# Kernel optimization log

Measured on AMD Instinct MI355X. Metric: run time of the kernel, lower is better.

## Reference

```python
import jax, jax.numpy as jnp
import numpy as np

N_NODES = 100000
N_EDGES = 3200000
N_GRAPHS = 256
IN_CH, EDGE_CH, HID, N_CLS = 11, 22, 64, 2


def setup_inputs() -> dict:
    key = jax.random.key(0)
    ks = jax.random.split(key, 16)
    s = 0.1
    return {
        "x": jax.random.normal(ks[0], (N_NODES, IN_CH), jnp.float32),
        "edge_attr": jax.random.normal(ks[1], (N_EDGES, EDGE_CH), jnp.float32),
        "edge_index": jax.random.randint(ks[2], (2, N_EDGES), 0, N_NODES, jnp.int64),
        "batch": jnp.sort(jax.random.randint(ks[3], (N_NODES,), 0, N_GRAPHS, jnp.int64)),
        # fc_edge: Linear(edge_ch -> in_ch)
        "we": jax.random.normal(ks[4], (IN_CH, EDGE_CH), jnp.float32) * s,
        "be": jnp.zeros((IN_CH,), jnp.float32),
        # SAGEConv i: lin_l (neighbors, with bias), lin_r (root, no bias)
        "l1w": jax.random.normal(ks[5], (HID, IN_CH), jnp.float32) * s,
        "l1b": jnp.zeros((HID,), jnp.float32),
        "r1w": jax.random.normal(ks[6], (HID, IN_CH), jnp.float32) * s,
        "l2w": jax.random.normal(ks[7], (HID, HID), jnp.float32) * s,
        "l2b": jnp.zeros((HID,), jnp.float32),
        "r2w": jax.random.normal(ks[8], (HID, HID), jnp.float32) * s,
        "l3w": jax.random.normal(ks[9], (HID, HID), jnp.float32) * s,
        "l3b": jnp.zeros((HID,), jnp.float32),
        "r3w": jax.random.normal(ks[10], (HID, HID), jnp.float32) * s,
        # final classifier
        "wf": jax.random.normal(ks[11], (N_CLS, HID), jnp.float32) * s,
        "bf": jnp.zeros((N_CLS,), jnp.float32),
    }


def _sage(x, src, dst, lw, lb, rw):
    # mean aggregation of source-node features at destination nodes
    agg = jax.ops.segment_sum(x[src], dst, num_segments=N_NODES)
    deg = jax.ops.segment_sum(jnp.ones((src.shape[0],), x.dtype), dst, num_segments=N_NODES)
    mean = agg / jnp.maximum(deg, 1.0)[:, None]
    return mean @ lw.T + lb + x @ rw.T


def reference(x, edge_attr, edge_index, batch, we, be,
              l1w, l1b, r1w, l2w, l2b, r2w, l3w, l3b, r3w, wf, bf):
    src, dst = edge_index[0], edge_index[1]
    # per-edge correction scatter-added to source nodes
    ec = edge_attr @ we.T + be                       # [E, in_ch]
    x = x.at[src].add(ec)                            # [N, in_ch]
    x = jax.nn.relu(_sage(x, src, dst, l1w, l1b, r1w))
    x = jax.nn.relu(_sage(x, src, dst, l2w, l2b, r2w))
    x = jax.nn.relu(_sage(x, src, dst, l3w, l3b, r3w))
    # global mean pool per graph
    psum = jax.ops.segment_sum(x, batch, num_segments=N_GRAPHS)
    cnt = jax.ops.segment_sum(jnp.ones((x.shape[0],), x.dtype), batch, num_segments=N_GRAPHS)
    pooled = psum / jnp.maximum(cnt, 1.0)[:, None]   # [G, hid]
    # dropout is identity in eval mode
    return pooled @ wf.T + bf                        # [G, num_classes]
```

## Files before the change

kernel.cpp:

```cpp
#include <hip/hip_runtime.h>
#include <stdint.h>

#define IN_CH 11
#define EDGE_CH 22
#define HID 64
#define N_CLS 2
#define N_GRAPHS 256

#define BK_SHIFT 8
#define BK_NODES 256
#define MAXBUK 512
#define L1_CHUNK 4096
#define L2_CAP 16384

#define SRC_SHIFT 22
#define DST_SHIFT 17

__global__ void prehist_kernel(const int* __restrict__ src, const int* __restrict__ dst,
                               int* __restrict__ bc_src, int* __restrict__ bc_dst,
                               int E, int nbuk) {
    __shared__ int h_s[MAXBUK], h_d[MAXBUK];
    int t = threadIdx.x;
    for (int i = t; i < MAXBUK; i += 256) { h_s[i] = 0; h_d[i] = 0; }
    __syncthreads();
    int per = (E + gridDim.x - 1) / gridDim.x;
    int lo = blockIdx.x * per, hi = min(E, lo + per);
    for (int i = lo + t; i < hi; i += 256) {
        atomicAdd(&h_s[src[i] >> BK_SHIFT], 1);
        atomicAdd(&h_d[dst[i] >> BK_SHIFT], 1);
    }
    __syncthreads();
    for (int i = t; i < nbuk; i += 256) {
        if (h_s[i]) atomicAdd(&bc_src[i], h_s[i]);
        if (h_d[i]) atomicAdd(&bc_dst[i], h_d[i]);
    }
}

__global__ void bucket_scan_kernel(const int* __restrict__ bc_src, const int* __restrict__ bc_dst,
                                   int* __restrict__ boff_src, int* __restrict__ boff_dst,
                                   int* __restrict__ gcur_src, int* __restrict__ gcur_dst,
                                   int* __restrict__ off_src, int* __restrict__ off_dst,
                                   int nbuk, int N, int E) {
    __shared__ int a[MAXBUK], b[MAXBUK];
    int t = threadIdx.x;
    int ca = (t < nbuk) ? bc_src[t] : 0;
    int cb = (t < nbuk) ? bc_dst[t] : 0;
    a[t] = ca; b[t] = cb;
    __syncthreads();
    for (int d = 1; d < MAXBUK; d <<= 1) {
        int ua = (t >= d) ? a[t - d] : 0;
        int ub = (t >= d) ? b[t - d] : 0;
        __syncthreads();
        a[t] += ua; b[t] += ub;
        __syncthreads();
    }
    if (t < nbuk) {
        int ea = a[t] - ca, eb = b[t] - cb;
        boff_src[t] = ea; gcur_src[t] = ea;
        boff_dst[t] = eb; gcur_dst[t] = eb;
    }
    if (t == 0) {
        boff_src[nbuk] = E; boff_dst[nbuk] = E;
        off_src[N] = E; off_dst[N] = E;
    }
}

__global__ void binscatter_kernel(const int* __restrict__ src, const int* __restrict__ dst,
                                  int* __restrict__ gcur_src, int* __restrict__ gcur_dst,
                                  uint32_t* __restrict__ bin_src, uint32_t* __restrict__ bin_dst,
                                  int E, int nbuk) {
    __shared__ int h_s[MAXBUK], h_d[MAXBUK];
    __shared__ int off_s[MAXBUK], off_d[MAXBUK];
    __shared__ int cur_s[MAXBUK], cur_d[MAXBUK];
    __shared__ int base_s[MAXBUK], base_d[MAXBUK];
    __shared__ uint32_t st_s[L1_CHUNK], st_d[L1_CHUNK];
    __shared__ unsigned short bk_s[L1_CHUNK], bk_d[L1_CHUNK];

    int t = threadIdx.x;
    int e0 = blockIdx.x * L1_CHUNK;
    int ecnt = min(E - e0, L1_CHUNK);

    h_s[t] = 0; h_d[t] = 0;
    __syncthreads();
    for (int i = t; i < ecnt; i += 512) {
        atomicAdd(&h_s[src[e0 + i] >> BK_SHIFT], 1);
        atomicAdd(&h_d[dst[e0 + i] >> BK_SHIFT], 1);
    }
    __syncthreads();
    int cs = h_s[t], cd = h_d[t];
    for (int d = 1; d < MAXBUK; d <<= 1) {
        int us = (t >= d) ? h_s[t - d] : 0;
        int ud = (t >= d) ? h_d[t - d] : 0;
        __syncthreads();
        h_s[t] += us; h_d[t] += ud;
        __syncthreads();
    }
    int ex_s = h_s[t] - cs, ex_d = h_d[t] - cd;
    off_s[t] = ex_s; cur_s[t] = ex_s;
    off_d[t] = ex_d; cur_d[t] = ex_d;
    if (cs > 0) base_s[t] = atomicAdd(&gcur_src[t], cs);
    if (cd > 0) base_d[t] = atomicAdd(&gcur_dst[t], cd);
    __syncthreads();
    for (int i = t; i < ecnt; i += 512) {
        int e = e0 + i;
        int s = src[e], d = dst[e];
        int bs = s >> BK_SHIFT, bd = d >> BK_SHIFT;
        int ps = atomicAdd(&cur_s[bs], 1);
        st_s[ps] = ((uint32_t)(s & (BK_NODES - 1)) << SRC_SHIFT) | (uint32_t)e;
        bk_s[ps] = (unsigned short)bs;
        int pd = atomicAdd(&cur_d[bd], 1);
        st_d[pd] = ((uint32_t)(d & (BK_NODES - 1)) << DST_SHIFT) | (uint32_t)s;
        bk_d[pd] = (unsigned short)bd;
    }
    __syncthreads();
    for (int i = t; i < ecnt; i += 512) {
        int b1 = bk_s[i];
        bin_src[base_s[b1] + i - off_s[b1]] = st_s[i];
        int b2 = bk_d[i];
        bin_dst[base_d[b2] + i - off_d[b2]] = st_d[i];
    }
}

__global__ void bucket_csr_kernel(const uint32_t* __restrict__ bin_src,
                                  const int* __restrict__ boff_src,
                                  int* __restrict__ src_edge, int* __restrict__ off_src,
                                  const uint32_t* __restrict__ bin_dst,
                                  const int* __restrict__ boff_dst,
                                  int* __restrict__ dst_srcid, int* __restrict__ off_dst,
                                  int nbuk, int N) {
    bool is_dst = blockIdx.x >= (unsigned)nbuk;
    int b = is_dst ? (blockIdx.x - nbuk) : blockIdx.x;
    const uint32_t* bin = is_dst ? bin_dst : bin_src;
    const int* boff = is_dst ? boff_dst : boff_src;
    int* outp = is_dst ? dst_srcid : src_edge;
    int* offo = is_dst ? off_dst : off_src;
    int shift = is_dst ? DST_SHIFT : SRC_SHIFT;
    uint32_t mask = (1u << shift) - 1;

    __shared__ int hist[BK_NODES];
    __shared__ int cursor[BK_NODES];
    __shared__ uint32_t stage[L2_CAP];

    int t = threadIdx.x;
    int base = boff[b];
    int cnt = boff[b + 1] - base;
    int n0 = b << BK_SHIFT;
    int NL = min(N - n0, BK_NODES);

    hist[t] = 0;
    __syncthreads();
    for (int i = t; i < cnt; i += 256) {
        atomicAdd(&hist[bin[base + i] >> shift], 1);
    }
    __syncthreads();
    int c = hist[t];
    for (int d = 1; d < BK_NODES; d <<= 1) {
        int u = (t >= d) ? hist[t - d] : 0;
        __syncthreads();
        hist[t] += u;
        __syncthreads();
    }
    int excl = hist[t] - c;
    cursor[t] = excl;
    if (t < NL) offo[n0 + t] = base + excl;
    __syncthreads();
    for (int i = t; i < cnt; i += 256) {
        uint32_t w = bin[base + i];
        int local = (int)(w >> shift);
        int pos = atomicAdd(&cursor[local], 1);
        uint32_t payload = w & mask;
        if (pos < L2_CAP) stage[pos] = payload;
        else outp[base + pos] = (int)payload;
    }
    __syncthreads();
    int lim = min(cnt, L2_CAP);
    for (int i = t; i < lim; i += 256) outp[base + i] = (int)stage[i];
}

__global__ void ea_gather_kernel(const float* __restrict__ ea,
                                 const int* __restrict__ off_src,
                                 const int* __restrict__ src_edge,
                                 float* __restrict__ agg_ea, int N) {
    int wave = (blockIdx.x * blockDim.x + threadIdx.x) >> 6;
    int lane = threadIdx.x & 63;
    if (wave >= N) return;
    int beg = off_src[wave], end = off_src[wave + 1];
    int j = lane >> 5;
    int c = lane & 31;
    float acc = 0.0f;
    if (c < EDGE_CH) {
        for (int i = beg + j; i < end; i += 2) {
            int e = src_edge[i];
            acc += ea[(long)e * EDGE_CH + c];
        }
    }
    acc += __shfl_xor(acc, 32, 64);
    if (lane < EDGE_CH) agg_ea[(long)wave * EDGE_CH + lane] = acc;
}

__global__ void x0_update_kernel(const float* __restrict__ x,
                                 const float* __restrict__ agg_ea,
                                 const int* __restrict__ off_src,
                                 const float* __restrict__ we,
                                 const float* __restrict__ be,
                                 float* __restrict__ x0, int N) {
    __shared__ float s_we[IN_CH * EDGE_CH];
    __shared__ float s_be[IN_CH];
    for (int i = threadIdx.x; i < IN_CH * EDGE_CH; i += blockDim.x) s_we[i] = we[i];
    if (threadIdx.x < IN_CH) s_be[threadIdx.x] = be[threadIdx.x];
    __syncthreads();
    int n = blockIdx.x * blockDim.x + threadIdx.x;
    if (n >= N) return;
    float a[EDGE_CH];
#pragma unroll
    for (int k = 0; k < EDGE_CH; ++k) a[k] = agg_ea[(long)n * EDGE_CH + k];
    float cnt = (float)(off_src[n + 1] - off_src[n]);
#pragma unroll
    for (int o = 0; o < IN_CH; ++o) {
        float acc = x[(long)n * IN_CH + o] + cnt * s_be[o];
#pragma unroll
        for (int k = 0; k < EDGE_CH; ++k) acc += a[k] * s_we[o * EDGE_CH + k];
        x0[(long)n * IN_CH + o] = acc;
    }
}

__global__ void agg11_kernel(const float* __restrict__ h,
                             const int* __restrict__ off_dst,
                             const int* __restrict__ srcid,
                             float* __restrict__ mean, int N) {
    int wave = (blockIdx.x * blockDim.x + threadIdx.x) >> 6;
    int lane = threadIdx.x & 63;
    if (wave >= N) return;
    int beg = off_dst[wave], end = off_dst[wave + 1];
    int j = lane >> 4;
    int c = lane & 15;
    float acc = 0.0f;
    if (c < IN_CH) {
        for (int i = beg + j; i < end; i += 4) {
            acc += h[(long)srcid[i] * IN_CH + c];
        }
    }
    acc += __shfl_xor(acc, 16, 64);
    acc += __shfl_xor(acc, 32, 64);
    if (lane < IN_CH) {
        float inv = 1.0f / fmaxf((float)(end - beg), 1.0f);
        mean[(long)wave * IN_CH + lane] = acc * inv;
    }
}

__global__ void agg64_kernel(const float* __restrict__ h,
                             const int* __restrict__ off_dst,
                             const int* __restrict__ srcid,
                             float* __restrict__ mean, int N) {
    int wave = (blockIdx.x * blockDim.x + threadIdx.x) >> 6;
    int lane = threadIdx.x & 63;
    if (wave >= N) return;
    int beg = off_dst[wave], end = off_dst[wave + 1];
    float a0 = 0.0f, a1 = 0.0f;
    int i = beg;
    for (; i + 1 < end; i += 2) {
        int s0 = srcid[i], s1 = srcid[i + 1];
        a0 += h[(long)s0 * HID + lane];
        a1 += h[(long)s1 * HID + lane];
    }
    if (i < end) a0 += h[(long)srcid[i] * HID + lane];
    float inv = 1.0f / fmaxf((float)(end - beg), 1.0f);
    mean[(long)wave * HID + lane] = (a0 + a1) * inv;
}

template <int CIN>
__global__ void update_kernel(const float* __restrict__ h_in,
                              const float* __restrict__ mean,
                              const float* __restrict__ lw,
                              const float* __restrict__ lb,
                              const float* __restrict__ rw,
                              float* __restrict__ h_out, int N) {
    __shared__ float s_lw[CIN][HID];
    __shared__ float s_rw[CIN][HID];
    __shared__ float s_lb[HID];
    __shared__ float s_hin[4][CIN];
    __shared__ float s_mean[4][CIN];
    for (int i = threadIdx.x; i < HID * CIN; i += blockDim.x) {
        int o = i / CIN, c = i % CIN;
        s_lw[c][o] = lw[i];
        s_rw[c][o] = rw[i];
    }
    if (threadIdx.x < HID) s_lb[threadIdx.x] = lb[threadIdx.x];
    __syncthreads();
    int sub = threadIdx.x >> 6, lane = threadIdx.x & 63;
    int groups = (N + 3) >> 2;
    for (int g = blockIdx.x; g < groups; g += gridDim.x) {
        int n = g * 4 + sub;
        bool valid = n < N;
        if (valid && lane < CIN) {
            s_hin[sub][lane] = h_in[(long)n * CIN + lane];
            s_mean[sub][lane] = mean[(long)n * CIN + lane];
        }
        __syncthreads();
        if (valid) {
            float acc = s_lb[lane];
#pragma unroll
            for (int c2 = 0; c2 < CIN; ++c2)
                acc += s_mean[sub][c2] * s_lw[c2][lane] + s_hin[sub][c2] * s_rw[c2][lane];
            h_out[(long)n * HID + lane] = fmaxf(acc, 0.0f);
        }
        __syncthreads();
    }
}

__global__ void pool_kernel(const float* __restrict__ h,
                            const int* __restrict__ batch,
                            float* __restrict__ psum,
                            float* __restrict__ pcnt,
                            int N, int chunk) {
    int lane = threadIdx.x;
    int n0 = blockIdx.x * chunk;
    int n1 = min(n0 + chunk, N);
    float acc = 0.0f, cnt = 0.0f;
    int cur = -1;
    for (int n = n0; n < n1; ++n) {
        int g = batch[n];
        if (g != cur) {
            if (cur >= 0) {
                atomicAdd(&psum[(long)cur * HID + lane], acc);
                if (lane == 0) atomicAdd(&pcnt[cur], cnt);
            }
            cur = g;
            acc = 0.0f;
            cnt = 0.0f;
        }
        acc += h[(long)n * HID + lane];
        cnt += 1.0f;
    }
    if (cur >= 0) {
        atomicAdd(&psum[(long)cur * HID + lane], acc);
        if (lane == 0) atomicAdd(&pcnt[cur], cnt);
    }
}

__global__ void final_kernel(const float* __restrict__ psum,
                             const float* __restrict__ pcnt,
                             const float* __restrict__ wf,
                             const float* __restrict__ bf,
                             float* __restrict__ out, int G) {
    int g = blockIdx.x * blockDim.x + threadIdx.x;
    if (g < G) {
        float inv = 1.0f / fmaxf(pcnt[g], 1.0f);
        float o0 = bf[0], o1 = bf[1];
#pragma unroll
        for (int c = 0; c < HID; ++c) {
            float p = psum[(long)g * HID + c] * inv;
            o0 += p * wf[c];
            o1 += p * wf[HID + c];
        }
        out[g * N_CLS + 0] = o0;
        out[g * N_CLS + 1] = o1;
    }
}

extern "C" void kernel_launch(void* const* d_in, const int* in_sizes, int n_in,
                              void* d_out, int out_size, void* d_ws, size_t ws_size,
                              hipStream_t stream) {
    const float* x         = (const float*)d_in[0];
    const float* edge_attr = (const float*)d_in[1];
    const int*   edge_idx  = (const int*)d_in[2];
    const int*   batch     = (const int*)d_in[3];
    const float* we  = (const float*)d_in[4];
    const float* be  = (const float*)d_in[5];
    const float* l1w = (const float*)d_in[6];
    const float* l1b = (const float*)d_in[7];
    const float* r1w = (const float*)d_in[8];
    const float* l2w = (const float*)d_in[9];
    const float* l2b = (const float*)d_in[10];
    const float* r2w = (const float*)d_in[11];
    const float* l3w = (const float*)d_in[12];
    const float* l3b = (const float*)d_in[13];
    const float* r3w = (const float*)d_in[14];
    const float* wf  = (const float*)d_in[15];
    const float* bf  = (const float*)d_in[16];

    const int E = in_sizes[2] / 2;
    const int N = in_sizes[3];
    const int* src = edge_idx;
    const int* dst = edge_idx + E;
    const int nbuk = (N + BK_NODES - 1) >> BK_SHIFT;

    char* p = (char*)d_ws;
    int* off_src   = (int*)p;            p += (size_t)(N + 1) * 4;
    int* off_dst   = (int*)p;            p += (size_t)(N + 1) * 4;
    int* bc_src    = (int*)p;            p += (size_t)MAXBUK * 4;
    int* bc_dst    = (int*)p;            p += (size_t)MAXBUK * 4;
    int* boff_src  = (int*)p;            p += (size_t)(MAXBUK + 1) * 4;
    int* boff_dst  = (int*)p;            p += (size_t)(MAXBUK + 1) * 4;
    int* gcur_src  = (int*)p;            p += (size_t)MAXBUK * 4;
    int* gcur_dst  = (int*)p;            p += (size_t)MAXBUK * 4;
    int* src_edge  = (int*)p;            p += (size_t)E * 4;
    int* dst_srcid = (int*)p;            p += (size_t)E * 4;
    float* x0      = (float*)p;          p += (size_t)N * IN_CH * 4;
    float* tmpM    = (float*)p;          p += (size_t)N * HID * 4;
    float* bufA    = (float*)p;          p += (size_t)N * HID * 4;
    float* bufB    = (float*)p;          p += (size_t)N * HID * 4;
    float* psum    = (float*)p;          p += (size_t)N_GRAPHS * HID * 4;
    float* pcnt    = (float*)p;          p += (size_t)N_GRAPHS * 4;

    uint32_t* bin_src = (uint32_t*)bufA;
    uint32_t* bin_dst = bin_src + E;

    const int NW = (N + 3) / 4;

    hipMemsetAsync(bc_src, 0, (size_t)MAXBUK * 2 * 4, stream);
    prehist_kernel<<<512, 256, 0, stream>>>(src, dst, bc_src, bc_dst, E, nbuk);
    bucket_scan_kernel<<<1, MAXBUK, 0, stream>>>(bc_src, bc_dst, boff_src, boff_dst,
                                                 gcur_src, gcur_dst, off_src, off_dst,
                                                 nbuk, N, E);
    binscatter_kernel<<<(E + L1_CHUNK - 1) / L1_CHUNK, 512, 0, stream>>>(
        src, dst, gcur_src, gcur_dst, bin_src, bin_dst, E, nbuk);
    bucket_csr_kernel<<<2 * nbuk, 256, 0, stream>>>(
        bin_src, boff_src, src_edge, off_src,
        bin_dst, boff_dst, dst_srcid, off_dst, nbuk, N);

    ea_gather_kernel<<<NW, 256, 0, stream>>>(edge_attr, off_src, src_edge, tmpM, N);
    x0_update_kernel<<<(N + 255) / 256, 256, 0, stream>>>(x, tmpM, off_src, we, be, x0, N);

    agg11_kernel<<<NW, 256, 0, stream>>>(x0, off_dst, dst_srcid, tmpM, N);
    update_kernel<IN_CH><<<2048, 256, 0, stream>>>(x0, tmpM, l1w, l1b, r1w, bufA, N);

    agg64_kernel<<<NW, 256, 0, stream>>>(bufA, off_dst, dst_srcid, tmpM, N);
    update_kernel<HID><<<2048, 256, 0, stream>>>(bufA, tmpM, l2w, l2b, r2w, bufB, N);

    agg64_kernel<<<NW, 256, 0, stream>>>(bufB, off_dst, dst_srcid, tmpM, N);
    update_kernel<HID><<<2048, 256, 0, stream>>>(bufB, tmpM, l3w, l3b, r3w, bufA, N);

    hipMemsetAsync(psum, 0, (size_t)(N_GRAPHS * HID + N_GRAPHS) * 4, stream);
    {
        int pb = 256;
        int chunk = (N + pb - 1) / pb;
        pool_kernel<<<pb, 64, 0, stream>>>(bufA, batch, psum, pcnt, N, chunk);
    }
    final_kernel<<<(N_GRAPHS + 255) / 256, 256, 0, stream>>>(psum, pcnt, wf, bf,
                                                             (float*)d_out, N_GRAPHS);
}
```

Baseline: 1.508 ms.

## Fuse edge-attr aggregation into bucket pass and fuse SAGE aggregation with update

Removes the src-side CSR build and instead aggregates edge attributes per source bucket directly in shared memory with LDS atomics, fused with the x0 linear update. Mean aggregation and the dense update of each SAGE layer are merged into a single kernel, so the intermediate mean buffer never goes through global memory. Gather loops are unrolled further for more memory-level parallelism, and the pool grid is widened. The trade-offs are heavy LDS atomic contention in the bucket kernel, fewer blocks for the hidden layers because of larger shared-memory use, and barriers inside the fused loops.

New measurement: 1.440 ms. 1.05x faster.

```diff
diff --git a/kernel.cpp b/kernel.cpp
--- a/kernel.cpp
+++ b/kernel.cpp
@@ -39,7 +39,7 @@
 __global__ void bucket_scan_kernel(const int* __restrict__ bc_src, const int* __restrict__ bc_dst,
                                    int* __restrict__ boff_src, int* __restrict__ boff_dst,
                                    int* __restrict__ gcur_src, int* __restrict__ gcur_dst,
-                                   int* __restrict__ off_src, int* __restrict__ off_dst,
+                                   int* __restrict__ off_dst,
                                    int nbuk, int N, int E) {
     __shared__ int a[MAXBUK], b[MAXBUK];
     int t = threadIdx.x;
@@ -61,7 +61,7 @@
     }
     if (t == 0) {
         boff_src[nbuk] = E; boff_dst[nbuk] = E;
-        off_src[N] = E; off_dst[N] = E;
+        off_dst[N] = E;
     }
 }
 
@@ -121,36 +121,26 @@
     }
 }
 
-__global__ void bucket_csr_kernel(const uint32_t* __restrict__ bin_src,
-                                  const int* __restrict__ boff_src,
-                                  int* __restrict__ src_edge, int* __restrict__ off_src,
-                                  const uint32_t* __restrict__ bin_dst,
+__global__ void bucket_csr_kernel(const uint32_t* __restrict__ bin_dst,
                                   const int* __restrict__ boff_dst,
                                   int* __restrict__ dst_srcid, int* __restrict__ off_dst,
                                   int nbuk, int N) {
-    bool is_dst = blockIdx.x >= (unsigned)nbuk;
-    int b = is_dst ? (blockIdx.x - nbuk) : blockIdx.x;
-    const uint32_t* bin = is_dst ? bin_dst : bin_src;
-    const int* boff = is_dst ? boff_dst : boff_src;
-    int* outp = is_dst ? dst_srcid : src_edge;
-    int* offo = is_dst ? off_dst : off_src;
-    int shift = is_dst ? DST_SHIFT : SRC_SHIFT;
-    uint32_t mask = (1u << shift) - 1;
-
+    int b = blockIdx.x;
     __shared__ int hist[BK_NODES];
     __shared__ int cursor[BK_NODES];
     __shared__ uint32_t stage[L2_CAP];
 
     int t = threadIdx.x;
-    int base = boff[b];
-    int cnt = boff[b + 1] - base;
+    int base = boff_dst[b];
+    int cnt = boff_dst[b + 1] - base;
     int n0 = b << BK_SHIFT;
     int NL = min(N - n0, BK_NODES);
+    uint32_t mask = (1u << DST_SHIFT) - 1;
 
     hist[t] = 0;
     __syncthreads();
     for (int i = t; i < cnt; i += 256) {
-        atomicAdd(&hist[bin[base + i] >> shift], 1);
+        atomicAdd(&hist[bin_dst[base + i] >> DST_SHIFT], 1);
     }
     __syncthreads();
     int c = hist[t];
@@ -162,147 +152,198 @@
     }
     int excl = hist[t] - c;
     cursor[t] = excl;
-    if (t < NL) offo[n0 + t] = base + excl;
+    if (t < NL) off_dst[n0 + t] = base + excl;
     __syncthreads();
     for (int i = t; i < cnt; i += 256) {
-        uint32_t w = bin[base + i];
-        int local = (int)(w >> shift);
+        uint32_t w = bin_dst[base + i];
+        int local = (int)(w >> DST_SHIFT);
         int pos = atomicAdd(&cursor[local], 1);
         uint32_t payload = w & mask;
         if (pos < L2_CAP) stage[pos] = payload;
-        else outp[base + pos] = (int)payload;
+        else dst_srcid[base + pos] = (int)payload;
     }
     __syncthreads();
     int lim = min(cnt, L2_CAP);
-    for (int i = t; i < lim; i += 256) outp[base + i] = (int)stage[i];
-}
-
-__global__ void ea_gather_kernel(const float* __restrict__ ea,
-                                 const int* __restrict__ off_src,
-                                 const int* __restrict__ src_edge,
-                                 float* __restrict__ agg_ea, int N) {
-    int wave = (blockIdx.x * blockDim.x + threadIdx.x) >> 6;
-    int lane = threadIdx.x & 63;
-    if (wave >= N) return;
-    int beg = off_src[wave], end = off_src[wave + 1];
-    int j = lane >> 5;
-    int c = lane & 31;
-    float acc = 0.0f;
-    if (c < EDGE_CH) {
-        for (int i = beg + j; i < end; i += 2) {
-            int e = src_edge[i];
-            acc += ea[(long)e * EDGE_CH + c];
-        }
-    }
-    acc += __shfl_xor(acc, 32, 64);
-    if (lane < EDGE_CH) agg_ea[(long)wave * EDGE_CH + lane] = acc;
-}
-
-__global__ void x0_update_kernel(const float* __restrict__ x,
-                                 const float* __restrict__ agg_ea,
-                                 const int* __restrict__ off_src,
+    for (int i = t; i < lim; i += 256) dst_srcid[base + i] = (int)stage[i];
+}
+
+__global__ void bucket_ea_kernel(const uint32_t* __restrict__ bin_src,
+                                 const int* __restrict__ boff_src,
+                                 const float* __restrict__ ea,
+                                 const float* __restrict__ x,
                                  const float* __restrict__ we,
                                  const float* __restrict__ be,
-                                 float* __restrict__ x0, int N) {
+                                 float* __restrict__ x0,
+                                 int nbuk, int N) {
+    __shared__ float s_ea[BK_NODES][EDGE_CH];
+    __shared__ int s_cnt[BK_NODES];
     __shared__ float s_we[IN_CH * EDGE_CH];
     __shared__ float s_be[IN_CH];
-    for (int i = threadIdx.x; i < IN_CH * EDGE_CH; i += blockDim.x) s_we[i] = we[i];
-    if (threadIdx.x < IN_CH) s_be[threadIdx.x] = be[threadIdx.x];
-    __syncthreads();
-    int n = blockIdx.x * blockDim.x + threadIdx.x;
-    if (n >= N) return;
-    float a[EDGE_CH];
-#pragma unroll
-    for (int k = 0; k < EDGE_CH; ++k) a[k] = agg_ea[(long)n * EDGE_CH + k];
-    float cnt = (float)(off_src[n + 1] - off_src[n]);
-#pragma unroll
-    for (int o = 0; o < IN_CH; ++o) {
-        float acc = x[(long)n * IN_CH + o] + cnt * s_be[o];
-#pragma unroll
-        for (int k = 0; k < EDGE_CH; ++k) acc += a[k] * s_we[o * EDGE_CH + k];
-        x0[(long)n * IN_CH + o] = acc;
-    }
-}
-
-__global__ void agg11_kernel(const float* __restrict__ h,
+    int t = threadIdx.x;
+    int b = blockIdx.x;
+    int base = boff_src[b];
+    int cnt = boff_src[b + 1] - base;
+    int n0 = b << BK_SHIFT;
+    int NL = min(N - n0, BK_NODES);
+
+    for (int i = t; i < IN_CH * EDGE_CH; i += 256) s_we[i] = we[i];
+    if (t < IN_CH) s_be[t] = be[t];
+    s_cnt[t] = 0;
+#pragma unroll
+    for (int c = 0; c < EDGE_CH; ++c) s_ea[t][c] = 0.0f;
+    __syncthreads();
+
+    const float2* ea2 = (const float2*)ea;
+    const uint32_t emask = (1u << SRC_SHIFT) - 1;
+    for (int i = t; i < cnt; i += 256) {
+        uint32_t w = bin_src[base + i];
+        int local = (int)(w >> SRC_SHIFT);
+        long eid = (long)(w & emask);
+        atomicAdd(&s_cnt[local], 1);
+        const float2* row = ea2 + eid * (EDGE_CH / 2);
+        float2 v[EDGE_CH / 2];
+#pragma unroll
+        for (int c = 0; c < EDGE_CH / 2; ++c) v[c] = row[c];
+#pragma unroll
+        for (int c = 0; c < EDGE_CH / 2; ++c) {
+            atomicAdd(&s_ea[local][2 * c], v[c].x);
+            atomicAdd(&s_ea[local][2 * c + 1], v[c].y);
+        }
+    }
+    __syncthreads();
+
+    if (t < NL) {
+        int n = n0 + t;
+        float cntf = (float)s_cnt[t];
+        float a[EDGE_CH];
+#pragma unroll
+        for (int c = 0; c < EDGE_CH; ++c) a[c] = s_ea[t][c];
+#pragma unroll
+        for (int o = 0; o < IN_CH; ++o) {
+            float acc = x[(long)n * IN_CH + o] + cntf * s_be[o];
+#pragma unroll
+            for (int c = 0; c < EDGE_CH; ++c) acc += a[c] * s_we[o * EDGE_CH + c];
+            x0[(long)n * IN_CH + o] = acc;
+        }
+    }
+}
+
+__global__ void layer1_fused(const float* __restrict__ x0,
                              const int* __restrict__ off_dst,
                              const int* __restrict__ srcid,
-                             float* __restrict__ mean, int N) {
-    int wave = (blockIdx.x * blockDim.x + threadIdx.x) >> 6;
-    int lane = threadIdx.x & 63;
-    if (wave >= N) return;
-    int beg = off_dst[wave], end = off_dst[wave + 1];
-    int j = lane >> 4;
-    int c = lane & 15;
-    float acc = 0.0f;
-    if (c < IN_CH) {
-        for (int i = beg + j; i < end; i += 4) {
-            acc += h[(long)srcid[i] * IN_CH + c];
-        }
-    }
-    acc += __shfl_xor(acc, 16, 64);
-    acc += __shfl_xor(acc, 32, 64);
-    if (lane < IN_CH) {
-        float inv = 1.0f / fmaxf((float)(end - beg), 1.0f);
-        mean[(long)wave * IN_CH + lane] = acc * inv;
-    }
-}
-
-__global__ void agg64_kernel(const float* __restrict__ h,
-                             const int* __restrict__ off_dst,
-                             const int* __restrict__ srcid,
-                             float* __restrict__ mean, int N) {
-    int wave = (blockIdx.x * blockDim.x + threadIdx.x) >> 6;
-    int lane = threadIdx.x & 63;
-    if (wave >= N) return;
-    int beg = off_dst[wave], end = off_dst[wave + 1];
-    float a0 = 0.0f, a1 = 0.0f;
-    int i = beg;
-    for (; i + 1 < end; i += 2) {
-        int s0 = srcid[i], s1 = srcid[i + 1];
-        a0 += h[(long)s0 * HID + lane];
-        a1 += h[(long)s1 * HID + lane];
-    }
-    if (i < end) a0 += h[(long)srcid[i] * HID + lane];
-    float inv = 1.0f / fmaxf((float)(end - beg), 1.0f);
-    mean[(long)wave * HID + lane] = (a0 + a1) * inv;
-}
-
-template <int CIN>
-__global__ void update_kernel(const float* __restrict__ h_in,
-                              const float* __restrict__ mean,
-                              const float* __restrict__ lw,
-                              const float* __restrict__ lb,
-                              const float* __restrict__ rw,
-                              float* __restrict__ h_out, int N) {
-    __shared__ float s_lw[CIN][HID];
-    __shared__ float s_rw[CIN][HID];
+                             const float* __restrict__ lw,
+                             const float* __restrict__ lb,
+                             const float* __restrict__ rw,
+                             float* __restrict__ h_out, int N) {
+    __shared__ float s_lw[IN_CH][HID];
+    __shared__ float s_rw[IN_CH][HID];
     __shared__ float s_lb[HID];
-    __shared__ float s_hin[4][CIN];
-    __shared__ float s_mean[4][CIN];
-    for (int i = threadIdx.x; i < HID * CIN; i += blockDim.x) {
-        int o = i / CIN, c = i % CIN;
+    __shared__ float s_mean[4][IN_CH];
+    __shared__ float s_hin[4][IN_CH];
+    for (int i = threadIdx.x; i < HID * IN_CH; i += 256) {
+        int o = i / IN_CH, c = i % IN_CH;
         s_lw[c][o] = lw[i];
         s_rw[c][o] = rw[i];
     }
     if (threadIdx.x < HID) s_lb[threadIdx.x] = lb[threadIdx.x];
-    __syncthreads();
+
+    int sub = threadIdx.x >> 6, lane = threadIdx.x & 63;
+    int j = lane >> 4, c = lane & 15;
+    int groups = (N + 3) >> 2;
+    for (int g = blockIdx.x; g < groups; g += gridDim.x) {
+        int n = g * 4 + sub;
+        bool valid = n < N;
+        int beg = 0, end = 0;
+        if (valid) { beg = off_dst[n]; end = off_dst[n + 1]; }
+        float a0 = 0.f, a1 = 0.f, a2 = 0.f, a3 = 0.f;
+        int i = beg;
+        if (valid && c < IN_CH) {
+            for (; i + 15 < end; i += 16) {
+                int s0 = srcid[i + j];
+                int s1 = srcid[i + j + 4];
+                int s2 = srcid[i + j + 8];
+                int s3 = srcid[i + j + 12];
+                a0 += x0[(long)s0 * IN_CH + c];
+                a1 += x0[(long)s1 * IN_CH + c];
+                a2 += x0[(long)s2 * IN_CH + c];
+                a3 += x0[(long)s3 * IN_CH + c];
+            }
+            for (; i + j < end; i += 4) a0 += x0[(long)srcid[i + j] * IN_CH + c];
+        }
+        float acc = (a0 + a1) + (a2 + a3);
+        acc += __shfl_xor(acc, 16, 64);
+        acc += __shfl_xor(acc, 32, 64);
+        if (valid && lane < IN_CH) {
+            float inv = 1.0f / fmaxf((float)(end - beg), 1.0f);
+            s_mean[sub][lane] = acc * inv;
+            s_hin[sub][lane] = x0[(long)n * IN_CH + lane];
+        }
+        __syncthreads();
+        if (valid) {
+            float oacc = s_lb[lane];
+#pragma unroll
+            for (int cc = 0; cc < IN_CH; ++cc)
+                oacc += s_mean[sub][cc] * s_lw[cc][lane] + s_hin[sub][cc] * s_rw[cc][lane];
+            h_out[(long)n * HID + lane] = fmaxf(oacc, 0.0f);
+        }
+        __syncthreads();
+    }
+}
+
+__global__ void layer_hid_fused(const float* __restrict__ h_in,
+                                const int* __restrict__ off_dst,
+                                const int* __restrict__ srcid,
+                                const float* __restrict__ lw,
+                                const float* __restrict__ lb,
+                                const float* __restrict__ rw,
+                                float* __restrict__ h_out, int N) {
+    __shared__ float s_lw[HID][HID];
+    __shared__ float s_rw[HID][HID];
+    __shared__ float s_lb[HID];
+    __shared__ float s_mean[4][HID];
+    __shared__ float s_hin[4][HID];
+    for (int i = threadIdx.x; i < HID * HID; i += 256) {
+        int o = i >> 6, c = i & 63;
+        s_lw[c][o] = lw[i];
+        s_rw[c][o] = rw[i];
+    }
+    if (threadIdx.x < HID) s_lb[threadIdx.x] = lb[threadIdx.x];
+
     int sub = threadIdx.x >> 6, lane = threadIdx.x & 63;
     int groups = (N + 3) >> 2;
     for (int g = blockIdx.x; g < groups; g += gridDim.x) {
         int n = g * 4 + sub;
         bool valid = n < N;
-        if (valid && lane < CIN) {
-            s_hin[sub][lane] = h_in[(long)n * CIN + lane];
-            s_mean[sub][lane] = mean[(long)n * CIN + lane];
-        }
-        __syncthreads();
+        int beg = 0, end = 0;
+        if (valid) { beg = off_dst[n]; end = off_dst[n + 1]; }
+        float a0 = 0.f, a1 = 0.f, a2 = 0.f, a3 = 0.f;
+        float a4 = 0.f, a5 = 0.f, a6 = 0.f, a7 = 0.f;
+        int i = beg;
+        for (; i + 7 < end; i += 8) {
+            int s0 = srcid[i], s1 = srcid[i + 1], s2 = srcid[i + 2], s3 = srcid[i + 3];
+            int s4 = srcid[i + 4], s5 = srcid[i + 5], s6 = srcid[i + 6], s7 = srcid[i + 7];
+            a0 += h_in[(long)s0 * HID + lane];
+            a1 += h_in[(long)s1 * HID + lane];
+            a2 += h_in[(long)s2 * HID + lane];
+            a3 += h_in[(long)s3 * HID + lane];
+            a4 += h_in[(long)s4 * HID + lane];
+            a5 += h_in[(long)s5 * HID + lane];
+            a6 += h_in[(long)s6 * HID + lane];
+            a7 += h_in[(long)s7 * HID + lane];
+        }
+        for (; i < end; ++i) a0 += h_in[(long)srcid[i] * HID + lane];
         if (valid) {
-            float acc = s_lb[lane];
-#pragma unroll
-            for (int c2 = 0; c2 < CIN; ++c2)
-                acc += s_mean[sub][c2] * s_lw[c2][lane] + s_hin[sub][c2] * s_rw[c2][lane];
-            h_out[(long)n * HID + lane] = fmaxf(acc, 0.0f);
+            float inv = 1.0f / fmaxf((float)(end - beg), 1.0f);
+            s_mean[sub][lane] = (((a0 + a1) + (a2 + a3)) + ((a4 + a5) + (a6 + a7))) * inv;
+            s_hin[sub][lane] = h_in[(long)n * HID + lane];
+        }
+        __syncthreads();
+        if (valid) {
+            float oacc = s_lb[lane];
+#pragma unroll
+            for (int cc = 0; cc < HID; ++cc)
+                oacc += s_mean[sub][cc] * s_lw[cc][lane] + s_hin[sub][cc] * s_rw[cc][lane];
+            h_out[(long)n * HID + lane] = fmaxf(oacc, 0.0f);
         }
         __syncthreads();
     }
@@ -386,7 +427,6 @@
     const int nbuk = (N + BK_NODES - 1) >> BK_SHIFT;
 
     char* p = (char*)d_ws;
-    int* off_src   = (int*)p;            p += (size_t)(N + 1) * 4;
     int* off_dst   = (int*)p;            p += (size_t)(N + 1) * 4;
     int* bc_src    = (int*)p;            p += (size_t)MAXBUK * 4;
     int* bc_dst    = (int*)p;            p += (size_t)MAXBUK * 4;
@@ -394,46 +434,38 @@
     int* boff_dst  = (int*)p;            p += (size_t)(MAXBUK + 1) * 4;
     int* gcur_src  = (int*)p;            p += (size_t)MAXBUK * 4;
     int* gcur_dst  = (int*)p;            p += (size_t)MAXBUK * 4;
-    int* src_edge  = (int*)p;            p += (size_t)E * 4;
     int* dst_srcid = (int*)p;            p += (size_t)E * 4;
     float* x0      = (float*)p;          p += (size_t)N * IN_CH * 4;
-    float* tmpM    = (float*)p;          p += (size_t)N * HID * 4;
     float* bufA    = (float*)p;          p += (size_t)N * HID * 4;
     float* bufB    = (float*)p;          p += (size_t)N * HID * 4;
     float* psum    = (float*)p;          p += (size_t)N_GRAPHS * HID * 4;
     float* pcnt    = (float*)p;          p += (size_t)N_GRAPHS * 4;
 
-    uint32_t* bin_src = (uint32_t*)bufA;
+    uint32_t* bin_src = (uint32_t*)bufB;
     uint32_t* bin_dst = bin_src + E;
-
-    const int NW = (N + 3) / 4;
 
     hipMemsetAsync(bc_src, 0, (size_t)MAXBUK * 2 * 4, stream);
     prehist_kernel<<<512, 256, 0, stream>>>(src, dst, bc_src, bc_dst, E, nbuk);
     bucket_scan_kernel<<<1, MAXBUK, 0, stream>>>(bc_src, bc_dst, boff_src, boff_dst,
-                                                 gcur_src, gcur_dst, off_src, off_dst,
+                                                 gcur_src, gcur_dst, off_dst,
                                                  nbuk, N, E);
     binscatter_kernel<<<(E + L1_CHUNK - 1) / L1_CHUNK, 512, 0, stream>>>(
         src, dst, gcur_src, gcur_dst, bin_src, bin_dst, E, nbuk);
-    bucket_csr_kernel<<<2 * nbuk, 256, 0, stream>>>(
-        bin_src, boff_src, src_edge, off_src,
+    bucket_csr_kernel<<<nbuk, 256, 0, stream>>>(
         bin_dst, boff_dst, dst_srcid, off_dst, nbuk, N);
 
-    ea_gather_kernel<<<NW, 256, 0, stream>>>(edge_attr, off_src, src_edge, tmpM, N);
-    x0_update_kernel<<<(N + 255) / 256, 256, 0, stream>>>(x, tmpM, off_src, we, be, x0, N);
-
-    agg11_kernel<<<NW, 256, 0, stream>>>(x0, off_dst, dst_srcid, tmpM, N);
-    update_kernel<IN_CH><<<2048, 256, 0, stream>>>(x0, tmpM, l1w, l1b, r1w, bufA, N);
-
-    agg64_kernel<<<NW, 256, 0, stream>>>(bufA, off_dst, dst_srcid, tmpM, N);
-    update_kernel<HID><<<2048, 256, 0, stream>>>(bufA, tmpM, l2w, l2b, r2w, bufB, N);
-
-    agg64_kernel<<<NW, 256, 0, stream>>>(bufB, off_dst, dst_srcid, tmpM, N);
-    update_kernel<HID><<<2048, 256, 0, stream>>>(bufB, tmpM, l3w, l3b, r3w, bufA, N);
+    bucket_ea_kernel<<<nbuk, 256, 0, stream>>>(
+        bin_src, boff_src, edge_attr, x, we, be, x0, nbuk, N);
+
+    layer1_fused<<<2048, 256, 0, stream>>>(x0, off_dst, dst_srcid, l1w, l1b, r1w, bufA, N);
+
+    layer_hid_fused<<<1024, 256, 0, stream>>>(bufA, off_dst, dst_srcid, l2w, l2b, r2w, bufB, N);
+
+    layer_hid_fused<<<1024, 256, 0, stream>>>(bufB, off_dst, dst_srcid, l3w, l3b, r3w, bufA, N);
 
     hipMemsetAsync(psum, 0, (size_t)(N_GRAPHS * HID + N_GRAPHS) * 4, stream);
     {
-        int pb = 256;
+        int pb = 1024;
         int chunk = (N + pb - 1) / pb;
         pool_kernel<<<pb, 64, 0, stream>>>(bufA, batch, psum, pcnt, N, chunk);
     }
```
